# Optimization experiments

Measured on AMD Instinct MI355X. Metric: run time of the kernel, lower is better.

Reference implementation:

```python
import jax, jax.numpy as jnp
import numpy as np

GRID_SIZE = 5
SPLINE_ORDER = 3
HIDDEN = 128
IN_FT = 768
BATCH = 32768

def make_grid():
    # uniform grid on [-1, 1] extended by spline_order knots on each side
    h = 2.0 / GRID_SIZE
    return (jnp.arange(-SPLINE_ORDER, GRID_SIZE + SPLINE_ORDER + 1, dtype=jnp.float32) * h - 1.0)

def b_splines(x, grid):
    # x: (B, in) -> bases: (B, in, GRID_SIZE + SPLINE_ORDER) via Cox-de-Boor recursion
    xe = x[..., None]                                  # (B, in, 1)
    bases = ((xe >= grid[:-1]) & (xe < grid[1:])).astype(x.dtype)
    for k in range(1, SPLINE_ORDER + 1):
        left = (xe - grid[:-(k + 1)]) / (grid[k:-1] - grid[:-(k + 1)]) * bases[..., :-1]
        right = (grid[k + 1:] - xe) / (grid[k + 1:] - grid[1:-k]) * bases[..., 1:]
        bases = left + right
    return bases

def kan_layer(x, base_w, spline_w, grid):
    # base_w: (out, in); spline_w: (out, in, G+k)
    B = x.shape[0]
    base_out = jax.nn.silu(x) @ base_w.T
    bas = b_splines(x, grid).reshape(B, -1)            # (B, in*(G+k))
    spline_out = bas @ spline_w.reshape(spline_w.shape[0], -1).T
    return base_out + spline_out

def setup_inputs() -> dict:
    key = jax.random.key(0)
    ks = jax.random.split(key, 8)
    nb = GRID_SIZE + SPLINE_ORDER  # 8 basis functions per edge
    return {
        "stm": jax.random.uniform(ks[0], (BATCH, IN_FT), dtype=jnp.float32),
        "nstm": jax.random.uniform(ks[1], (BATCH, IN_FT), dtype=jnp.float32),
        "ft_w": jax.random.normal(ks[2], (HIDDEN, IN_FT), dtype=jnp.float32) * 0.02,
        "ft_b": jnp.zeros((HIDDEN,), dtype=jnp.float32),
        "kan1_base_w": jax.random.normal(ks[3], (HIDDEN, 2 * HIDDEN), dtype=jnp.float32) * 0.05,
        "kan1_spline_w": jax.random.normal(ks[4], (HIDDEN, 2 * HIDDEN, nb), dtype=jnp.float32) * 0.05,
        "kan2_base_w": jax.random.normal(ks[5], (1, HIDDEN), dtype=jnp.float32) * 0.05,
        "kan2_spline_w": jax.random.normal(ks[6], (1, HIDDEN, nb), dtype=jnp.float32) * 0.05,
    }

def reference(stm, nstm, ft_w, ft_b, kan1_base_w, kan1_spline_w, kan2_base_w, kan2_spline_w):
    grid = make_grid()
    stm_h = stm @ ft_w.T + ft_b
    nstm_h = nstm @ ft_w.T + ft_b
    hidden = jnp.concatenate([stm_h, nstm_h], axis=1)   # (B, 2*HIDDEN)
    hidden = kan_layer(hidden, kan1_base_w, kan1_spline_w, grid)
    out = kan_layer(hidden, kan2_base_w, kan2_spline_w, grid)
    return jax.nn.sigmoid(out)
```

## Files before the change

kernel.cpp:

```cpp
#include <hip/hip_runtime.h>
#include <hip/hip_bf16.h>
#include <math.h>
#include <stdint.h>

typedef __attribute__((ext_vector_type(8))) short bf16x8;
typedef __attribute__((ext_vector_type(4))) float f32x4;

__device__ __forceinline__ uint32_t pack2(float a, float b) {
    union { __hip_bfloat162 h2; uint32_t u; } c;
    c.h2 = __float22bfloat162_rn(make_float2(a, b));
    return c.u;
}
__device__ __forceinline__ unsigned short f2bf(float f) {
    union { __hip_bfloat16 h; unsigned short u; } c;
    c.h = __float2bfloat16(f);
    return c.u;
}
__device__ __forceinline__ float bf2f(unsigned short h) {
    union { uint32_t u; float f; } c; c.u = ((uint32_t)h) << 16;
    return c.f;
}
__device__ __forceinline__ float silu_f(float x) {
    return x / (1.0f + __expf(-x));
}

__device__ __forceinline__ void bspline8(float x, float* __restrict__ b) {
    const float tt = (x + 2.2f) * 2.5f;
#pragma unroll
    for (int v = 0; v < 8; ++v) {
        float y = fabsf(tt - (float)(v + 2));
        float p = fmaxf(2.0f - y, 0.0f);
        float q = fmaxf(1.0f - y, 0.0f);
        b[v] = (p * p * p - 4.0f * q * q * q) * (1.0f / 6.0f);
    }
}

__device__ __forceinline__ void gload16(const void* g, void* l) {
    __builtin_amdgcn_global_load_lds(
        (const __attribute__((address_space(1))) void*)g,
        (__attribute__((address_space(3))) void*)l, 16, 0, 0);
}

__global__ __launch_bounds__(256) void prep_ftw(const float* __restrict__ ftw,
                                                unsigned short* __restrict__ Wb) {
    const int idx = blockIdx.x * 256 + threadIdx.x;
    Wb[idx] = f2bf(ftw[idx]);
}

__global__ __launch_bounds__(256) void prep_bp(const float* __restrict__ bw,
                                               const float* __restrict__ sw,
                                               unsigned short* __restrict__ Bp) {
    const int idx = blockIdx.x * 256 + threadIdx.x;
    const int n = idx >> 12;
    const int k = idx & 4095;
    const int f = k >> 4;
    const int v = k & 15;
    float val = 0.f;
    if (v == 0) val = bw[n * 256 + f];
    else if (v <= 8) val = sw[(size_t)(n * 256 + f) * 8 + (v - 1)];
    Bp[idx] = f2bf(val);
}

__global__ __launch_bounds__(512, 4) void kan_fused(
        const float* __restrict__ stm, const float* __restrict__ nstm,
        const unsigned short* __restrict__ Wb, const float* __restrict__ bias,
        const unsigned short* __restrict__ Bp,
        const float* __restrict__ w2b, const float* __restrict__ w2s,
        float* __restrict__ out) {
    __shared__ alignas(16) char lds[81920];
    char* smA  = lds;
    char* smB  = lds + 16384;
    char* smHT = lds + 49152;

    const int r0 = blockIdx.x * 64;
    const int t = threadIdx.x;
    const int l = t & 63, w = t >> 6;
    const int fr = l & 15, h = l >> 4;
    const int wr = w >> 2, wc = w & 3;

    const int arow = t >> 3;
    const int acol = (t & 7) * 16;
    const uint32_t adst0 = (uint32_t)arow * 256u +
        ((uint32_t)(((t & 7) * 2) ^ (arow & 15)) << 4);
    const uint32_t adst1 = (uint32_t)arow * 256u +
        ((uint32_t)(((t & 7) * 2 + 1) ^ (arow & 15)) << 4);
    const int gidx = w * 4;

    f32x4 acc[2][2];
#pragma unroll
    for (int mt = 0; mt < 2; ++mt)
#pragma unroll
        for (int nt = 0; nt < 2; ++nt) acc[mt][nt] = (f32x4){0.f, 0.f, 0.f, 0.f};

    float4 regY[4], regZ[4];

#define FT_ISSUE(REG, TK)                                                      \
    {                                                                          \
        const float* __restrict__ Ap = ((TK) >= 6) ? nstm : stm;               \
        const int kk = ((TK) % 6) * 128;                                       \
        _Pragma("unroll") for (int q = 0; q < 4; ++q)                          \
            REG[q] = *reinterpret_cast<const float4*>(                         \
                &Ap[(size_t)(r0 + arow) * 768 + kk + acol + q * 4]);           \
    }

#define FT_WRITE(REG)                                                          \
    {                                                                          \
        int4 w0, w1;                                                           \
        w0.x = (int)pack2(REG[0].x, REG[0].y);                                 \
        w0.y = (int)pack2(REG[0].z, REG[0].w);                                 \
        w0.z = (int)pack2(REG[1].x, REG[1].y);                                 \
        w0.w = (int)pack2(REG[1].z, REG[1].w);                                 \
        w1.x = (int)pack2(REG[2].x, REG[2].y);                                 \
        w1.y = (int)pack2(REG[2].z, REG[2].w);                                 \
        w1.z = (int)pack2(REG[3].x, REG[3].y);                                 \
        w1.w = (int)pack2(REG[3].z, REG[3].w);                                 \
        *reinterpret_cast<int4*>(smA + adst0) = w0;                            \
        *reinterpret_cast<int4*>(smA + adst1) = w1;                            \
    }

#define GLOADB_FT(K0)                                                          \
    _Pragma("unroll") for (int j = 0; j < 4; ++j) {                            \
        const int col = (gidx + j) * 4 + (l >> 4);                             \
        gload16(&Wb[(size_t)col * 768 + (K0) + (((l & 15) ^ (col & 15)) << 3)],\
                smB + (gidx + j) * 1024);                                      \
    }

#define GEMM_STEP()                                                            \
    _Pragma("unroll") for (int ks = 0; ks < 4; ++ks) {                         \
        bf16x8 a[2], b[2];                                                     \
        _Pragma("unroll") for (int mt = 0; mt < 2; ++mt) {                     \
            const uint32_t row = (uint32_t)(wr * 32 + mt * 16 + fr);           \
            a[mt] = *reinterpret_cast<const bf16x8*>(                          \
                smA + row * 256u +                                             \
                (((uint32_t)(ks * 4 + h) ^ (row & 15u)) << 4));                \
        }                                                                      \
        _Pragma("unroll") for (int nt = 0; nt < 2; ++nt) {                     \
            const uint32_t col = (uint32_t)(wc * 32 + nt * 16 + fr);           \
            b[nt] = *reinterpret_cast<const bf16x8*>(                          \
                smB + col * 256u +                                             \
                (((uint32_t)(ks * 4 + h) ^ (col & 15u)) << 4));                \
        }                                                                      \
        _Pragma("unroll") for (int mt = 0; mt < 2; ++mt)                       \
            _Pragma("unroll") for (int nt = 0; nt < 2; ++nt)                   \
                acc[mt][nt] = __builtin_amdgcn_mfma_f32_16x16x32_bf16(         \
                    a[mt], b[nt], acc[mt][nt], 0, 0, 0);                       \
    }

#define DUMP_H(SO)                                                             \
    _Pragma("unroll") for (int nt = 0; nt < 2; ++nt) {                         \
        const int col = wc * 32 + nt * 16 + fr;                                \
        const float bv = bias[col];                                            \
        const int feat = (SO) + col;                                           \
        _Pragma("unroll") for (int mt = 0; mt < 2; ++mt) {                     \
            const int rowb = wr * 32 + mt * 16 + h * 4;                        \
            int2 o;                                                            \
            o.x = (int)pack2(acc[mt][nt][0] + bv, acc[mt][nt][1] + bv);        \
            o.y = (int)pack2(acc[mt][nt][2] + bv, acc[mt][nt][3] + bv);        \
            const uint32_t db = (uint32_t)feat * 128u +                        \
                ((uint32_t)((rowb >> 3) ^ (feat & 7)) << 4) +                  \
                (uint32_t)(rowb & 7) * 2u;                                     \
            *reinterpret_cast<int2*>(smHT + db) = o;                           \
            acc[mt][nt] = (f32x4){0.f, 0.f, 0.f, 0.f};                         \
        }                                                                      \
    }

#define LGKM_BAR()                                                             \
    asm volatile("s_waitcnt lgkmcnt(0)" ::: "memory");                         \
    __builtin_amdgcn_sched_barrier(0);                                         \
    __builtin_amdgcn_s_barrier();

    FT_ISSUE(regY, 0);
    FT_ISSUE(regZ, 1);
#pragma unroll 1
    for (int pp = 0; pp < 6; ++pp) {
        FT_WRITE(regY);
        GLOADB_FT(((2 * pp) % 6) * 128);
        __builtin_amdgcn_sched_barrier(0);
        if (pp < 5) {
            FT_ISSUE(regY, 2 * pp + 2);
            asm volatile("s_waitcnt vmcnt(4)" ::: "memory");
        } else {
            asm volatile("s_waitcnt vmcnt(0)" ::: "memory");
        }
        asm volatile("s_waitcnt lgkmcnt(0)" ::: "memory");
        __builtin_amdgcn_sched_barrier(0);
        __builtin_amdgcn_s_barrier();
        __builtin_amdgcn_s_setprio(1);
        GEMM_STEP();
        __builtin_amdgcn_s_setprio(0);
        LGKM_BAR();
        FT_WRITE(regZ);
        GLOADB_FT(((2 * pp + 1) % 6) * 128);
        __builtin_amdgcn_sched_barrier(0);
        if (pp < 5) {
            FT_ISSUE(regZ, 2 * pp + 3);
            asm volatile("s_waitcnt vmcnt(4)" ::: "memory");
        } else {
            asm volatile("s_waitcnt vmcnt(0)" ::: "memory");
        }
        asm volatile("s_waitcnt lgkmcnt(0)" ::: "memory");
        __builtin_amdgcn_sched_barrier(0);
        __builtin_amdgcn_s_barrier();
        __builtin_amdgcn_s_setprio(1);
        GEMM_STEP();
        __builtin_amdgcn_s_setprio(0);
        if (pp == 2) { DUMP_H(0); }
        if (pp == 5) { DUMP_H(128); }
        LGKM_BAR();
    }

#pragma unroll 1
    for (int jb = 0; jb < 32; ++jb) {
#pragma unroll
        for (int j = 0; j < 4; ++j) {
            const int col = (gidx + j) * 4 + (l >> 4);
            gload16(&Bp[(size_t)col * 4096 + jb * 128 +
                        (((l & 15) ^ (col & 15)) << 3)],
                    smB + (gidx + j) * 1024);
        }
        __builtin_amdgcn_sched_barrier(0);
        {
            const int feat = jb * 8 + w;
            const unsigned short xv = *reinterpret_cast<const unsigned short*>(
                smHT + (uint32_t)feat * 128u +
                ((uint32_t)((l >> 3) ^ (feat & 7)) << 4) + (uint32_t)(l & 7) * 2u);
            const float x = bf2f(xv);
            float bs[8];
            bspline8(x, bs);
            const uint32_t pw0 = pack2(silu_f(x), bs[0]);
            const uint32_t pw1 = pack2(bs[1], bs[2]);
            const uint32_t pw2 = pack2(bs[3], bs[4]);
            const uint32_t pw3 = pack2(bs[5], bs[6]);
            const uint32_t pw4 = pack2(bs[7], 0.f);
            const uint32_t d0 = (uint32_t)l * 256u +
                ((uint32_t)((2 * w) ^ (l & 15)) << 4);
            const uint32_t d1 = (uint32_t)l * 256u +
                ((uint32_t)((2 * w + 1) ^ (l & 15)) << 4);
            *reinterpret_cast<int4*>(smA + d0) =
                make_int4((int)pw0, (int)pw1, (int)pw2, (int)pw3);
            *reinterpret_cast<int4*>(smA + d1) = make_int4((int)pw4, 0, 0, 0);
        }
        asm volatile("s_waitcnt vmcnt(0) lgkmcnt(0)" ::: "memory");
        __builtin_amdgcn_sched_barrier(0);
        __builtin_amdgcn_s_barrier();
        __builtin_amdgcn_s_setprio(1);
        GEMM_STEP();
        __builtin_amdgcn_s_setprio(0);
        LGKM_BAR();
    }

    unsigned short* smH2 = (unsigned short*)lds;
#pragma unroll
    for (int mt = 0; mt < 2; ++mt)
#pragma unroll
        for (int nt = 0; nt < 2; ++nt) {
            const int col = wc * 32 + nt * 16 + fr;
#pragma unroll
            for (int j = 0; j < 4; ++j) {
                const int row = wr * 32 + mt * 16 + h * 4 + j;
                smH2[row * 136 + col] = f2bf(acc[mt][nt][j]);
            }
        }
    __syncthreads();
    const int row2 = t >> 3, qd = t & 7;
    float sum = 0.f;
#pragma unroll 4
    for (int i = 0; i < 16; ++i) {
        const int j = qd * 16 + ((i + qd * 2) & 15);
        const float x = bf2f(smH2[row2 * 136 + j]);
        float bs[8];
        bspline8(x, bs);
        const float4 s0 = *reinterpret_cast<const float4*>(&w2s[j * 8]);
        const float4 s1 = *reinterpret_cast<const float4*>(&w2s[j * 8 + 4]);
        float s = silu_f(x) * w2b[j];
        s += bs[0] * s0.x + bs[1] * s0.y + bs[2] * s0.z + bs[3] * s0.w;
        s += bs[4] * s1.x + bs[5] * s1.y + bs[6] * s1.z + bs[7] * s1.w;
        sum += s;
    }
    sum += __shfl_xor(sum, 1, 64);
    sum += __shfl_xor(sum, 2, 64);
    sum += __shfl_xor(sum, 4, 64);
    if (qd == 0) out[r0 + row2] = 1.0f / (1.0f + __expf(-sum));
}

extern "C" void kernel_launch(void* const* d_in, const int* in_sizes, int n_in,
                              void* d_out, int out_size, void* d_ws, size_t ws_size,
                              hipStream_t stream) {
    const float* stm  = (const float*)d_in[0];
    const float* nstm = (const float*)d_in[1];
    const float* ft_w = (const float*)d_in[2];
    const float* ft_b = (const float*)d_in[3];
    const float* k1bw = (const float*)d_in[4];
    const float* k1sw = (const float*)d_in[5];
    const float* k2bw = (const float*)d_in[6];
    const float* k2sw = (const float*)d_in[7];
    float* out = (float*)d_out;

    char* ws = (char*)d_ws;
    unsigned short* Wb = (unsigned short*)ws;
    unsigned short* Bp = (unsigned short*)(ws + 196608);

    prep_ftw<<<384, 256, 0, stream>>>(ft_w, Wb);
    prep_bp<<<2048, 256, 0, stream>>>(k1bw, k1sw, Bp);
    kan_fused<<<512, 512, 0, stream>>>(stm, nstm, Wb, ft_b, Bp, k2bw, k2sw, out);
}
```

Before: 105.6 us.

## Load B operands directly to registers and double-buffer spline expansion

Replaces the LDS staging of the B operand (global_load_lds into smB, then LDS reads) with direct global-to-register loads into a per-wave bf16x8 fragment array. The spline/SiLU expansion stage gains a second LDS buffer, so the next feature block is expanded while the current one is multiplied. This shrinks LDS from 80KB to 64KB. It also drops the explicit vmcnt waits, leaving the compiler to place them. Each wave now fetches its own B columns from global/L2 instead of sharing them through LDS, and register pressure rises.

```diff
diff --git a/kernel.cpp b/kernel.cpp
--- a/kernel.cpp
+++ b/kernel.cpp
@@ -33,12 +33,6 @@
         float q = fmaxf(1.0f - y, 0.0f);
         b[v] = (p * p * p - 4.0f * q * q * q) * (1.0f / 6.0f);
     }
-}
-
-__device__ __forceinline__ void gload16(const void* g, void* l) {
-    __builtin_amdgcn_global_load_lds(
-        (const __attribute__((address_space(1))) void*)g,
-        (__attribute__((address_space(3))) void*)l, 16, 0, 0);
 }
 
 __global__ __launch_bounds__(256) void prep_ftw(const float* __restrict__ ftw,
@@ -67,10 +61,10 @@
         const unsigned short* __restrict__ Bp,
         const float* __restrict__ w2b, const float* __restrict__ w2s,
         float* __restrict__ out) {
-    __shared__ alignas(16) char lds[81920];
+    __shared__ alignas(16) char lds[65536];
     char* smA  = lds;
-    char* smB  = lds + 16384;
-    char* smHT = lds + 49152;
+    char* phi1 = lds + 16384;
+    char* smHT = lds + 32768;
 
     const int r0 = blockIdx.x * 64;
     const int t = threadIdx.x;
@@ -84,7 +78,6 @@
         ((uint32_t)(((t & 7) * 2) ^ (arow & 15)) << 4);
     const uint32_t adst1 = (uint32_t)arow * 256u +
         ((uint32_t)(((t & 7) * 2 + 1) ^ (arow & 15)) << 4);
-    const int gidx = w * 4;
 
     f32x4 acc[2][2];
 #pragma unroll
@@ -93,6 +86,7 @@
         for (int nt = 0; nt < 2; ++nt) acc[mt][nt] = (f32x4){0.f, 0.f, 0.f, 0.f};
 
     float4 regY[4], regZ[4];
+    bf16x8 bf[2][4];
 
 #define FT_ISSUE(REG, TK)                                                      \
     {                                                                          \
@@ -118,32 +112,27 @@
         *reinterpret_cast<int4*>(smA + adst1) = w1;                            \
     }
 
-#define GLOADB_FT(K0)                                                          \
-    _Pragma("unroll") for (int j = 0; j < 4; ++j) {                            \
-        const int col = (gidx + j) * 4 + (l >> 4);                             \
-        gload16(&Wb[(size_t)col * 768 + (K0) + (((l & 15) ^ (col & 15)) << 3)],\
-                smB + (gidx + j) * 1024);                                      \
-    }
-
-#define GEMM_STEP()                                                            \
+#define LOADB(PTR, KTOT, K0)                                                   \
+    _Pragma("unroll") for (int nt = 0; nt < 2; ++nt)                           \
+        _Pragma("unroll") for (int ks = 0; ks < 4; ++ks) {                     \
+            const int col = wc * 32 + nt * 16 + fr;                            \
+            bf[nt][ks] = *reinterpret_cast<const bf16x8*>(                     \
+                &PTR[(size_t)col * (KTOT) + (K0) + ks * 32 + h * 8]);          \
+        }
+
+#define GEMM_STEP(PHI)                                                         \
     _Pragma("unroll") for (int ks = 0; ks < 4; ++ks) {                         \
-        bf16x8 a[2], b[2];                                                     \
+        bf16x8 a[2];                                                           \
         _Pragma("unroll") for (int mt = 0; mt < 2; ++mt) {                     \
             const uint32_t row = (uint32_t)(wr * 32 + mt * 16 + fr);           \
             a[mt] = *reinterpret_cast<const bf16x8*>(                          \
-                smA + row * 256u +                                             \
+                (PHI) + row * 256u +                                           \
                 (((uint32_t)(ks * 4 + h) ^ (row & 15u)) << 4));                \
-        }                                                                      \
-        _Pragma("unroll") for (int nt = 0; nt < 2; ++nt) {                     \
-            const uint32_t col = (uint32_t)(wc * 32 + nt * 16 + fr);           \
-            b[nt] = *reinterpret_cast<const bf16x8*>(                          \
-                smB + col * 256u +                                             \
-                (((uint32_t)(ks * 4 + h) ^ (col & 15u)) << 4));                \
         }                                                                      \
         _Pragma("unroll") for (int mt = 0; mt < 2; ++mt)                       \
             _Pragma("unroll") for (int nt = 0; nt < 2; ++nt)                   \
                 acc[mt][nt] = __builtin_amdgcn_mfma_f32_16x16x32_bf16(         \
-                    a[mt], b[nt], acc[mt][nt], 0, 0, 0);                       \
+                    a[mt], bf[nt][ks], acc[mt][nt], 0, 0, 0);                  \
     }
 
 #define DUMP_H(SO)                                                             \
@@ -164,89 +153,75 @@
         }                                                                      \
     }
 
-#define LGKM_BAR()                                                             \
+#define EXPAND(DST, JF)                                                        \
+    {                                                                          \
+        const int feat = (JF) * 8 + w;                                         \
+        const unsigned short xv = *reinterpret_cast<const unsigned short*>(    \
+            smHT + (uint32_t)feat * 128u +                                     \
+            ((uint32_t)((l >> 3) ^ (feat & 7)) << 4) + (uint32_t)(l & 7) * 2u);\
+        const float x = bf2f(xv);                                              \
+        float bs[8];                                                           \
+        bspline8(x, bs);                                                       \
+        const uint32_t pw0 = pack2(silu_f(x), bs[0]);                          \
+        const uint32_t pw1 = pack2(bs[1], bs[2]);                              \
+        const uint32_t pw2 = pack2(bs[3], bs[4]);                              \
+        const uint32_t pw3 = pack2(bs[5], bs[6]);                              \
+        const uint32_t pw4 = pack2(bs[7], 0.f);                                \
+        const uint32_t d0 = (uint32_t)l * 256u +                               \
+            ((uint32_t)((2 * w) ^ (l & 15)) << 4);                             \
+        const uint32_t d1 = (uint32_t)l * 256u +                               \
+            ((uint32_t)((2 * w + 1) ^ (l & 15)) << 4);                         \
+        *reinterpret_cast<int4*>((DST) + d0) =                                 \
+            make_int4((int)pw0, (int)pw1, (int)pw2, (int)pw3);                 \
+        *reinterpret_cast<int4*>((DST) + d1) = make_int4((int)pw4, 0, 0, 0);   \
+    }
+
+#define BAR1()                                                                 \
     asm volatile("s_waitcnt lgkmcnt(0)" ::: "memory");                         \
     __builtin_amdgcn_sched_barrier(0);                                         \
     __builtin_amdgcn_s_barrier();
+#define BAR2()                                                                 \
+    __builtin_amdgcn_sched_barrier(0);                                         \
+    __builtin_amdgcn_s_barrier();                                              \
+    __builtin_amdgcn_sched_barrier(0);
 
     FT_ISSUE(regY, 0);
     FT_ISSUE(regZ, 1);
 #pragma unroll 1
     for (int pp = 0; pp < 6; ++pp) {
         FT_WRITE(regY);
-        GLOADB_FT(((2 * pp) % 6) * 128);
-        __builtin_amdgcn_sched_barrier(0);
-        if (pp < 5) {
-            FT_ISSUE(regY, 2 * pp + 2);
-            asm volatile("s_waitcnt vmcnt(4)" ::: "memory");
-        } else {
-            asm volatile("s_waitcnt vmcnt(0)" ::: "memory");
-        }
-        asm volatile("s_waitcnt lgkmcnt(0)" ::: "memory");
-        __builtin_amdgcn_sched_barrier(0);
-        __builtin_amdgcn_s_barrier();
+        if (pp < 5) FT_ISSUE(regY, 2 * pp + 2);
+        LOADB(Wb, 768, ((2 * pp) % 6) * 128);
+        BAR1();
         __builtin_amdgcn_s_setprio(1);
-        GEMM_STEP();
+        GEMM_STEP(smA);
         __builtin_amdgcn_s_setprio(0);
-        LGKM_BAR();
+        BAR2();
         FT_WRITE(regZ);
-        GLOADB_FT(((2 * pp + 1) % 6) * 128);
-        __builtin_amdgcn_sched_barrier(0);
-        if (pp < 5) {
-            FT_ISSUE(regZ, 2 * pp + 3);
-            asm volatile("s_waitcnt vmcnt(4)" ::: "memory");
-        } else {
-            asm volatile("s_waitcnt vmcnt(0)" ::: "memory");
-        }
-        asm volatile("s_waitcnt lgkmcnt(0)" ::: "memory");
-        __builtin_amdgcn_sched_barrier(0);
-        __builtin_amdgcn_s_barrier();
+        if (pp < 5) FT_ISSUE(regZ, 2 * pp + 3);
+        LOADB(Wb, 768, ((2 * pp + 1) % 6) * 128);
+        BAR1();
         __builtin_amdgcn_s_setprio(1);
-        GEMM_STEP();
+        GEMM_STEP(smA);
         __builtin_amdgcn_s_setprio(0);
         if (pp == 2) { DUMP_H(0); }
         if (pp == 5) { DUMP_H(128); }
-        LGKM_BAR();
-    }
-
+        asm volatile("s_waitcnt lgkmcnt(0)" ::: "memory");
+        BAR2();
+    }
+
+    EXPAND(smA, 0);
 #pragma unroll 1
     for (int jb = 0; jb < 32; ++jb) {
-#pragma unroll
-        for (int j = 0; j < 4; ++j) {
-            const int col = (gidx + j) * 4 + (l >> 4);
-            gload16(&Bp[(size_t)col * 4096 + jb * 128 +
-                        (((l & 15) ^ (col & 15)) << 3)],
-                    smB + (gidx + j) * 1024);
-        }
-        __builtin_amdgcn_sched_barrier(0);
-        {
-            const int feat = jb * 8 + w;
-            const unsigned short xv = *reinterpret_cast<const unsigned short*>(
-                smHT + (uint32_t)feat * 128u +
-                ((uint32_t)((l >> 3) ^ (feat & 7)) << 4) + (uint32_t)(l & 7) * 2u);
-            const float x = bf2f(xv);
-            float bs[8];
-            bspline8(x, bs);
-            const uint32_t pw0 = pack2(silu_f(x), bs[0]);
-            const uint32_t pw1 = pack2(bs[1], bs[2]);
-            const uint32_t pw2 = pack2(bs[3], bs[4]);
-            const uint32_t pw3 = pack2(bs[5], bs[6]);
-            const uint32_t pw4 = pack2(bs[7], 0.f);
-            const uint32_t d0 = (uint32_t)l * 256u +
-                ((uint32_t)((2 * w) ^ (l & 15)) << 4);
-            const uint32_t d1 = (uint32_t)l * 256u +
-                ((uint32_t)((2 * w + 1) ^ (l & 15)) << 4);
-            *reinterpret_cast<int4*>(smA + d0) =
-                make_int4((int)pw0, (int)pw1, (int)pw2, (int)pw3);
-            *reinterpret_cast<int4*>(smA + d1) = make_int4((int)pw4, 0, 0, 0);
-        }
-        asm volatile("s_waitcnt vmcnt(0) lgkmcnt(0)" ::: "memory");
-        __builtin_amdgcn_sched_barrier(0);
-        __builtin_amdgcn_s_barrier();
+        char* phiC = (jb & 1) ? phi1 : smA;
+        char* phiN = (jb & 1) ? smA : phi1;
+        LOADB(Bp, 4096, jb * 128);
+        if (jb < 31) EXPAND(phiN, jb + 1);
+        BAR1();
         __builtin_amdgcn_s_setprio(1);
-        GEMM_STEP();
+        GEMM_STEP(phiC);
         __builtin_amdgcn_s_setprio(0);
-        LGKM_BAR();
+        BAR2();
     }
 
     unsigned short* smH2 = (unsigned short*)lds;
```

After: 200.4 us. 1.9x slower.

## Load KAN1 weight fragments directly into registers in MFMA layout

Applied to the files above, without the earlier changes.

The prep kernel now stores the KAN layer-1 weights pre-arranged in the per-lane MFMA B-fragment order. The spline GEMM loop loads these fragments straight from global memory into registers instead of staging them through LDS with global_load_lds. This removes the LDS B reads and part of the LDS traffic per step. In exchange it adds 8 vector registers per thread and global load latency on the critical path, since no prefetch is shown, and the waitcnt now relies on the compiler to wait on the vmcnt before the MFMAs.

```diff
diff --git a/kernel.cpp b/kernel.cpp
--- a/kernel.cpp
+++ b/kernel.cpp
@@ -47,24 +47,25 @@
     Wb[idx] = f2bf(ftw[idx]);
 }
 
-__global__ __launch_bounds__(256) void prep_bp(const float* __restrict__ bw,
-                                               const float* __restrict__ sw,
-                                               unsigned short* __restrict__ Bp) {
+__global__ __launch_bounds__(256) void prep_bpf(const float* __restrict__ bw,
+                                                const float* __restrict__ sw,
+                                                unsigned short* __restrict__ BpF) {
     const int idx = blockIdx.x * 256 + threadIdx.x;
-    const int n = idx >> 12;
-    const int k = idx & 4095;
-    const int f = k >> 4;
-    const int v = k & 15;
+    const int e = idx & 7, l = (idx >> 3) & 63, ks = (idx >> 9) & 3;
+    const int nt = (idx >> 11) & 1, wc = (idx >> 12) & 3, jb = idx >> 14;
+    const int col = wc * 32 + nt * 16 + (l & 15);
+    const int k = jb * 128 + ks * 32 + (l >> 4) * 8 + e;
+    const int f = k >> 4, v = k & 15;
     float val = 0.f;
-    if (v == 0) val = bw[n * 256 + f];
-    else if (v <= 8) val = sw[(size_t)(n * 256 + f) * 8 + (v - 1)];
-    Bp[idx] = f2bf(val);
+    if (v == 0) val = bw[col * 256 + f];
+    else if (v <= 8) val = sw[(size_t)(col * 256 + f) * 8 + (v - 1)];
+    BpF[idx] = f2bf(val);
 }
 
 __global__ __launch_bounds__(512, 4) void kan_fused(
         const float* __restrict__ stm, const float* __restrict__ nstm,
         const unsigned short* __restrict__ Wb, const float* __restrict__ bias,
-        const unsigned short* __restrict__ Bp,
+        const unsigned short* __restrict__ BpF,
         const float* __restrict__ w2b, const float* __restrict__ w2s,
         float* __restrict__ out) {
     __shared__ alignas(16) char lds[81920];
@@ -93,6 +94,7 @@
         for (int nt = 0; nt < 2; ++nt) acc[mt][nt] = (f32x4){0.f, 0.f, 0.f, 0.f};
 
     float4 regY[4], regZ[4];
+    bf16x8 bf[2][4];
 
 #define FT_ISSUE(REG, TK)                                                      \
     {                                                                          \
@@ -125,7 +127,17 @@
                 smB + (gidx + j) * 1024);                                      \
     }
 
-#define GEMM_STEP()                                                            \
+#define LOADF(JB)                                                              \
+    {                                                                          \
+        const unsigned short* __restrict__ fb =                                \
+            BpF + (size_t)(JB) * 16384 + wc * 4096 + l * 8;                    \
+        _Pragma("unroll") for (int nt = 0; nt < 2; ++nt)                       \
+            _Pragma("unroll") for (int ks = 0; ks < 4; ++ks)                   \
+                bf[nt][ks] = *reinterpret_cast<const bf16x8*>(                 \
+                    fb + nt * 2048 + ks * 512);                                \
+    }
+
+#define GEMM_STEP_LDS()                                                        \
     _Pragma("unroll") for (int ks = 0; ks < 4; ++ks) {                         \
         bf16x8 a[2], b[2];                                                     \
         _Pragma("unroll") for (int mt = 0; mt < 2; ++mt) {                     \
@@ -146,6 +158,21 @@
                     a[mt], b[nt], acc[mt][nt], 0, 0, 0);                       \
     }
 
+#define GEMM_STEP_REG()                                                        \
+    _Pragma("unroll") for (int ks = 0; ks < 4; ++ks) {                         \
+        bf16x8 a[2];                                                           \
+        _Pragma("unroll") for (int mt = 0; mt < 2; ++mt) {                     \
+            const uint32_t row = (uint32_t)(wr * 32 + mt * 16 + fr);           \
+            a[mt] = *reinterpret_cast<const bf16x8*>(                          \
+                smA + row * 256u +                                             \
+                (((uint32_t)(ks * 4 + h) ^ (row & 15u)) << 4));                \
+        }                                                                      \
+        _Pragma("unroll") for (int mt = 0; mt < 2; ++mt)                       \
+            _Pragma("unroll") for (int nt = 0; nt < 2; ++nt)                   \
+                acc[mt][nt] = __builtin_amdgcn_mfma_f32_16x16x32_bf16(         \
+                    a[mt], bf[nt][ks], acc[mt][nt], 0, 0, 0);                  \
+    }
+
 #define DUMP_H(SO)                                                             \
     _Pragma("unroll") for (int nt = 0; nt < 2; ++nt) {                         \
         const int col = wc * 32 + nt * 16 + fr;                                \
@@ -186,7 +213,7 @@
         __builtin_amdgcn_sched_barrier(0);
         __builtin_amdgcn_s_barrier();
         __builtin_amdgcn_s_setprio(1);
-        GEMM_STEP();
+        GEMM_STEP_LDS();
         __builtin_amdgcn_s_setprio(0);
         LGKM_BAR();
         FT_WRITE(regZ);
@@ -202,7 +229,7 @@
         __builtin_amdgcn_sched_barrier(0);
         __builtin_amdgcn_s_barrier();
         __builtin_amdgcn_s_setprio(1);
-        GEMM_STEP();
+        GEMM_STEP_LDS();
         __builtin_amdgcn_s_setprio(0);
         if (pp == 2) { DUMP_H(0); }
         if (pp == 5) { DUMP_H(128); }
@@ -211,13 +238,7 @@
 
 #pragma unroll 1
     for (int jb = 0; jb < 32; ++jb) {
-#pragma unroll
-        for (int j = 0; j < 4; ++j) {
-            const int col = (gidx + j) * 4 + (l >> 4);
-            gload16(&Bp[(size_t)col * 4096 + jb * 128 +
-                        (((l & 15) ^ (col & 15)) << 3)],
-                    smB + (gidx + j) * 1024);
-        }
+        LOADF(jb);
         __builtin_amdgcn_sched_barrier(0);
         {
             const int feat = jb * 8 + w;
@@ -240,11 +261,11 @@
                 make_int4((int)pw0, (int)pw1, (int)pw2, (int)pw3);
             *reinterpret_cast<int4*>(smA + d1) = make_int4((int)pw4, 0, 0, 0);
         }
-        asm volatile("s_waitcnt vmcnt(0) lgkmcnt(0)" ::: "memory");
+        asm volatile("s_waitcnt lgkmcnt(0)" ::: "memory");
         __builtin_amdgcn_sched_barrier(0);
         __builtin_amdgcn_s_barrier();
         __builtin_amdgcn_s_setprio(1);
-        GEMM_STEP();
+        GEMM_STEP_REG();
         __builtin_amdgcn_s_setprio(0);
         LGKM_BAR();
     }
@@ -297,10 +318,10 @@
     float* out = (float*)d_out;
 
     char* ws = (char*)d_ws;
-    unsigned short* Wb = (unsigned short*)ws;
-    unsigned short* Bp = (unsigned short*)(ws + 196608);
+    unsigned short* Wb  = (unsigned short*)ws;
+    unsigned short* BpF = (unsigned short*)(ws + 196608);
 
     prep_ftw<<<384, 256, 0, stream>>>(ft_w, Wb);
-    prep_bp<<<2048, 256, 0, stream>>>(k1bw, k1sw, Bp);
-    kan_fused<<<512, 512, 0, stream>>>(stm, nstm, Wb, ft_b, Bp, k2bw, k2sw, out);
-}
+    prep_bpf<<<2048, 256, 0, stream>>>(k1bw, k1sw, BpF);
+    kan_fused<<<512, 512, 0, stream>>>(stm, nstm, Wb, ft_b, BpF, k2bw, k2sw, out);
+}
```

Result: no change. 104.3 us, median of 2 (-1.2%).
